# Performance work log

Hardware: AMD Instinct MI355X
Metric: run time of the kernel (lower is better)

## Reference

```python
import jax, jax.numpy as jnp
import numpy as np

NBATCH, NATOM, NEIGH = 16, 512, 64
NTYPE, NWAVE, NIPSIN, NORBIT = 4, 8, 3, 128
CUTOFF = 5.0
NPAIR = NATOM * NEIGH  # neighbor pairs per configuration


def _make_index_para(nipsin):
    # [0, 1,1,1, 2,...(9 times)] -> angular-order label per channel
    parts = [np.zeros(1, np.int32)]
    for i in range(1, nipsin):
        parts.append(np.full(3 ** i, i, np.int32))
    return jnp.asarray(np.concatenate(parts))


def setup_inputs() -> dict:
    key = jax.random.key(0)
    ks = jax.random.split(key, 10)
    cart = jax.random.uniform(ks[0], (NBATCH, NATOM, 3), jnp.float32) * 6.0
    numatoms = jnp.full((NBATCH,), NATOM, dtype=jnp.int32)
    species = jax.random.randint(ks[1], (NBATCH * NATOM,), 0, NTYPE).astype(jnp.int32)
    atom_index = jax.random.randint(ks[2], (2, NBATCH, NPAIR), 0, NATOM).astype(jnp.int32)
    shifts = jnp.zeros((NBATCH, NPAIR, 3), jnp.float32)  # all pairs valid (pass >-1e10 check)
    # learned parameters / buffers
    rs = jnp.tile(jnp.linspace(0.5, 4.0, NWAVE, dtype=jnp.float32)[None, :], (NTYPE, 1))
    inta = -(jax.random.uniform(ks[3], (NTYPE, NWAVE), jnp.float32) * 0.9 + 0.1)
    params = jnp.ones((NTYPE, NWAVE), jnp.float32) / float(NEIGH)
    hyper = jax.random.normal(ks[4], (1, NIPSIN, NWAVE, NORBIT), jnp.float32) * (1.0 / np.sqrt(NWAVE))
    index_para = _make_index_para(NIPSIN)
    return {"cart": cart, "numatoms": numatoms, "species": species,
            "atom_index": atom_index, "shifts": shifts,
            "rs": rs, "inta": inta, "params": params, "hyper": hyper,
            "index_para": index_para, "cutoff": CUTOFF}


def _angular(dist_vec, f_cut, nipsin):
    # dist_vec: [N,3], f_cut: [N] -> [L, N] with L = 1 + 3 + ... + 3^(nipsin-1)
    dv = dist_vec.T  # [3, N]
    orb = f_cut[None, :]
    parts = [orb]
    for _ in range(1, nipsin):
        orb = (orb[:, None, :] * dv[None, :, :]).reshape(-1, dv.shape[1])
        parts.append(orb)
    return jnp.concatenate(parts, axis=0)


def reference(cart, numatoms, species, atom_index, shifts, rs, inta, params, hyper, index_para, cutoff):
    nbatch, natom, _ = cart.shape
    totnatom = nbatch * natom
    cart_ = cart.reshape(totnatom, 3)
    # offset per-config neighbor indices to global atom ids
    offs = (jnp.arange(nbatch, dtype=atom_index.dtype) * natom)[None, :, None]
    idx12 = (atom_index + offs).reshape(2, -1)  # [2, Npairs]
    dist_vec = cart_[idx12[0]] - cart_[idx12[1]] + shifts.reshape(-1, 3)  # [Npairs,3]
    distances = jnp.linalg.norm(dist_vec, axis=-1)  # [Npairs]
    sp_j = species[idx12[1]]
    f_cut = jnp.square(0.5 * jnp.cos(distances * (jnp.pi / cutoff)) + 0.5)
    # per-pair gaussian radial basis, gathered by neighbor element type
    radial = jnp.exp(inta[sp_j] * jnp.square(distances[:, None] - rs[sp_j]))  # [Npairs, nwave]
    ang = _angular(dist_vec, f_cut, NIPSIN)  # [L, Npairs]
    orbital = ang.T[:, :, None] * radial[:, None, :]  # [Npairs, L, nwave]
    orb_coeff = params[species]  # [totnatom, nwave] (all species >= 0)
    # iteration 0 (ocmod_list is empty, so no refinement loop)
    worb = orbital * orb_coeff[idx12[1]][:, None, :]  # [Npairs, L, nwave]
    sum_worb = jax.ops.segment_sum(worb, idx12[0], num_segments=totnatom)  # [totnatom, L, nwave]
    hp = hyper[0][index_para]  # [L, nwave, norbit]
    hw = jnp.einsum('ijk,jkm->ijm', sum_worb, hp)  # [totnatom, L, norbit]
    density = jnp.sum(jnp.square(hw), axis=1)  # [totnatom, norbit]
    return density
```

## Files before the change

kernel.cpp:

```cpp
#include <hip/hip_runtime.h>
#include <hip/hip_bf16.h>

#define NBATCH  16
#define NATOM   512
#define NEIGH   64
#define NPAIR   (NATOM * NEIGH)
#define TOTPAIR (NBATCH * NPAIR)
#define TOTATOM (NBATCH * NATOM)
#define NTYPE   4
#define NWAVE   8
#define NL      13
#define NORBIT  128
#define CAP     128
#define NSUB    8
#define SUBCAP  40
#define PAIRS_PER_SUB (NPAIR / NSUB)

#define AST     136
#define S2ST    40

#define WS_COUNT_OFF 0
#define WS_HFRAG_OFF 262144
#define WS_PAY_OFF   278528


typedef __attribute__((ext_vector_type(8))) short  short8;
typedef __attribute__((ext_vector_type(4))) float  f32x4;

static __device__ inline unsigned short f2bf(float f) {
    unsigned u = __builtin_bit_cast(unsigned, f);
    u += 0x7FFFu + ((u >> 16) & 1u);
    return (unsigned short)(u >> 16);
}
static __device__ inline float bf2f(unsigned short h) {
    unsigned u = ((unsigned)h) << 16;
    return __builtin_bit_cast(float, u);
}

__global__ __launch_bounds__(512) void fill_kernel(
    const float* __restrict__ cart,
    const int*   __restrict__ species,
    const int*   __restrict__ atom_index,
    const float* __restrict__ shifts,
    const float* __restrict__ rs,
    const float* __restrict__ inta,
    const float* __restrict__ params,
    const float* __restrict__ cutoff_p,
    const float* __restrict__ hyper,
    int*            __restrict__ count,
    unsigned short* __restrict__ hfrag,
    unsigned short* __restrict__ payload)
{
    const int bid = blockIdx.x;
    const int b   = bid >> 3;
    const int s   = bid & 7;
    const int tid = threadIdx.x;

    __shared__ int   s_cnt[NATOM];
    __shared__ float s_tab[3 * NTYPE * NWAVE];

    if (tid < NTYPE * NWAVE) {
        s_tab[tid]                     = rs[tid];
        s_tab[NTYPE * NWAVE + tid]     = inta[tid];
        s_tab[2 * NTYPE * NWAVE + tid] = params[tid];
    }
    s_cnt[tid] = 0;

    if (bid < 16 && tid < 64) {
        const int hs = bid >> 3, n = bid & 7, lane = tid;
        const int q = lane >> 4, col = n * 16 + (lane & 15);
#pragma unroll
        for (int j = 0; j < 8; ++j) {
            int k = q * 8 + j;
            float f = (k < 24)
                ? hyper[(k >> 3) * (NWAVE * NORBIT) + (k & 7) * NORBIT + col]
                : 0.0f;
            unsigned short hi = f2bf(f);
            unsigned short v  = hs ? f2bf(f - bf2f(hi)) : hi;
            hfrag[((size_t)(bid * 64 + lane)) * 8 + j] = v;
        }
    }
    __syncthreads();

    const float pic = 3.14159265358979323846f / cutoff_p[0];
    const int pbase = b * NPAIR;

    for (int it = 0; it < PAIRS_PER_SUB / 512; ++it) {
        int pl = s * PAIRS_PER_SUB + it * 512 + tid;
        int p  = pbase + pl;
        int il = atom_index[p];
        int j  = atom_index[TOTPAIR + p] + (b << 9);
        int i  = il + (b << 9);

        float dx = cart[3 * i + 0] - cart[3 * j + 0] + shifts[3 * p + 0];
        float dy = cart[3 * i + 1] - cart[3 * j + 1] + shifts[3 * p + 1];
        float dz = cart[3 * i + 2] - cart[3 * j + 2] + shifts[3 * p + 2];
        float d  = sqrtf(dx * dx + dy * dy + dz * dz);

        float c  = 0.5f * __cosf(d * pic) + 0.5f;
        float fc = c * c;

        int slot = atomicAdd(&s_cnt[il], 1);
        if (slot < SUBCAP) {
            float a1 = fc * dx, a2 = fc * dy, a3 = fc * dz;
            short8 v0, v1, v2, v3;
            v0[0] = (short)f2bf(fc);
            v0[1] = (short)f2bf(a1);      v0[2] = (short)f2bf(a2);
            v0[3] = (short)f2bf(a3);
            v0[4] = (short)f2bf(a1 * dx); v0[5] = (short)f2bf(a1 * dy);
            v0[6] = (short)f2bf(a1 * dz); v0[7] = (short)f2bf(a2 * dx);
            v1[0] = (short)f2bf(a2 * dy); v1[1] = (short)f2bf(a2 * dz);
            v1[2] = (short)f2bf(a3 * dx); v1[3] = (short)f2bf(a3 * dy);
            v1[4] = (short)f2bf(a3 * dz);
            v1[5] = 0; v1[6] = 0; v1[7] = 0;

            int sp = species[j];
#pragma unroll
            for (int w = 0; w < NWAVE; ++w) {
                float tt = d - s_tab[sp * NWAVE + w];
                float rp = __expf(s_tab[NTYPE * NWAVE + sp * NWAVE + w] * tt * tt)
                         * s_tab[2 * NTYPE * NWAVE + sp * NWAVE + w];
                unsigned short hi = f2bf(rp);
                v2[w] = (short)hi;
                v3[w] = (short)f2bf(rp - bf2f(hi));
            }

            short8* dst = (short8*)(payload +
                (((size_t)((b * NATOM + il) * NSUB + s)) * SUBCAP + slot) * 32);
            dst[0] = v0; dst[1] = v1; dst[2] = v2; dst[3] = v3;
        }
    }
    __syncthreads();

    count[s * TOTATOM + (b * NATOM + tid)] = s_cnt[tid];
}

__global__ __launch_bounds__(128) void gather_kernel(
    const int*            __restrict__ count,
    const unsigned short* __restrict__ payload,
    const unsigned short* __restrict__ hfrag,
    float*                __restrict__ out)
{
    const int i      = blockIdx.x;
    const int tid    = threadIdx.x;
    const int lane   = tid & 63;
    const int waveId = tid >> 6;

    __shared__ __attribute__((aligned(16))) unsigned short s_A[16 * AST];
    __shared__ __attribute__((aligned(16))) unsigned short s_B[16 * AST];
    __shared__ __attribute__((aligned(16))) unsigned short s_S2[16 * S2ST];
    __shared__ int s_cv[NSUB];
    __shared__ int s_off[NSUB + 1];

    short8 hb[4], lb[4];
#pragma unroll
    for (int t = 0; t < 4; ++t) {
        int n = waveId * 4 + t;
        hb[t] = *(const short8*)&hfrag[((size_t)(n * 64 + lane)) * 8];
        lb[t] = *(const short8*)&hfrag[((size_t)((8 + n) * 64 + lane)) * 8];
    }

    if (tid < NSUB) {
        int c = count[tid * TOTATOM + i];
        s_cv[tid] = c < SUBCAP ? c : SUBCAP;
    }
    for (int e = tid; e < 16 * S2ST; e += 128) s_S2[e] = 0;
    __syncthreads();

    if (tid == 0) {
        int o = 0;
#pragma unroll
        for (int s2 = 0; s2 < NSUB; ++s2) { s_off[s2] = o; o += s_cv[s2]; }
        s_off[NSUB] = o;
    }
    __syncthreads();

    int total = s_off[NSUB];
    if (total > CAP) total = CAP;
    const int T = (total + 31) >> 5;

    if (tid < total) {
        const int k = tid;
        int s2 = 0;
#pragma unroll
        for (int t = 1; t < NSUB; ++t)
            if (k >= s_off[t]) s2 = t;
        const short8* rec = (const short8*)(payload +
            (((size_t)(i * NSUB + s2)) * SUBCAP + (k - s_off[s2])) * 32);
        short8 v0 = rec[0], v1 = rec[1], v2 = rec[2], v3 = rec[3];

        s_A[0 * AST + k]  = (unsigned short)v0[0];
        s_A[1 * AST + k]  = (unsigned short)v0[1];
        s_A[2 * AST + k]  = (unsigned short)v0[2];
        s_A[3 * AST + k]  = (unsigned short)v0[3];
        s_A[4 * AST + k]  = (unsigned short)v0[4];
        s_A[5 * AST + k]  = (unsigned short)v0[5];
        s_A[6 * AST + k]  = (unsigned short)v0[6];
        s_A[7 * AST + k]  = (unsigned short)v0[7];
        s_A[8 * AST + k]  = (unsigned short)v1[0];
        s_A[9 * AST + k]  = (unsigned short)v1[1];
        s_A[10 * AST + k] = (unsigned short)v1[2];
        s_A[11 * AST + k] = (unsigned short)v1[3];
        s_A[12 * AST + k] = (unsigned short)v1[4];
#pragma unroll
        for (int w = 0; w < NWAVE; ++w) {
            s_B[w * AST + k]       = (unsigned short)v2[w];
            s_B[(8 + w) * AST + k] = (unsigned short)v3[w];
        }
    }
    if (T > 0 && total < T * 32) {
        int tb = (T - 1) << 5;
        for (int e = tid; e < 16 * 32; e += 128) {
            int row = e >> 5, k = tb + (e & 31);
            if (k >= total) { s_A[row * AST + k] = 0; s_B[row * AST + k] = 0; }
        }
    }
    __syncthreads();

    if (waveId == 0) {
        const int m = lane & 15, q = lane >> 4;
        f32x4 acc = {0.f, 0.f, 0.f, 0.f};
        for (int t = 0; t < T; ++t) {
            short8 af  = *(const short8*)&s_A[m * AST + t * 32 + q * 8];
            short8 bhf = *(const short8*)&s_B[m * AST + t * 32 + q * 8];
            short8 blf = *(const short8*)&s_B[(m + 8) * AST + t * 32 + q * 8];
            acc = __builtin_amdgcn_mfma_f32_16x16x32_bf16(af, bhf, acc, 0, 0, 0);
            acc = __builtin_amdgcn_mfma_f32_16x16x32_bf16(af, blf, acc, 0, 0, 0);
        }
        if (m < 8) {
#pragma unroll
            for (int reg = 0; reg < 4; ++reg) {
                int l = q * 4 + reg;
                if (l < 13) {
                    int ip = (l == 0) ? 0 : ((l < 4) ? 1 : 2);
                    s_S2[l * S2ST + ip * 8 + m] = f2bf(acc[reg]);
                }
            }
        }
    }
    __syncthreads();

    {
        const int m = lane & 15, q = lane >> 4;
        short8 sf = *(const short8*)&s_S2[m * S2ST + q * 8];
#pragma unroll
        for (int t = 0; t < 4; ++t) {
            f32x4 acc = {0.f, 0.f, 0.f, 0.f};
            acc = __builtin_amdgcn_mfma_f32_16x16x32_bf16(sf, hb[t], acc, 0, 0, 0);
            acc = __builtin_amdgcn_mfma_f32_16x16x32_bf16(sf, lb[t], acc, 0, 0, 0);
            float part = 0.f;
#pragma unroll
            for (int reg = 0; reg < 4; ++reg) {
                int l = q * 4 + reg;
                if (l < 13) part += acc[reg] * acc[reg];
            }
            part += __shfl_xor(part, 16);
            part += __shfl_xor(part, 32);
            if (lane < 16)
                out[(size_t)i * NORBIT + (waveId * 4 + t) * 16 + lane] = part;
        }
    }
}

extern "C" void kernel_launch(void* const* d_in, const int* in_sizes, int n_in,
                              void* d_out, int out_size, void* d_ws, size_t ws_size,
                              hipStream_t stream) {
    const float* cart       = (const float*)d_in[0];
    const int*   species    = (const int*)  d_in[2];
    const int*   atom_index = (const int*)  d_in[3];
    const float* shifts     = (const float*)d_in[4];
    const float* rs         = (const float*)d_in[5];
    const float* inta       = (const float*)d_in[6];
    const float* params     = (const float*)d_in[7];
    const float* hyper      = (const float*)d_in[8];
    const float* cutoff_p   = (const float*)d_in[10];

    int*            count   = (int*)((char*)d_ws + WS_COUNT_OFF);
    unsigned short* hfrag   = (unsigned short*)((char*)d_ws + WS_HFRAG_OFF);
    unsigned short* payload = (unsigned short*)((char*)d_ws + WS_PAY_OFF);
    float* out = (float*)d_out;

    fill_kernel<<<NBATCH * NSUB, 512, 0, stream>>>(
        cart, species, atom_index, shifts, rs, inta, params, cutoff_p, hyper,
        count, hfrag, payload);

    gather_kernel<<<TOTATOM, 128, 0, stream>>>(count, payload, hfrag, out);
}
```

Before: 114.6 us.

## Process one atom per wave in gather and split fill into 16 sub-blocks

The fill kernel now uses 16 sub-blocks per batch with a smaller per-sub capacity, which doubles the fill grid so more CUs take part. The gather kernel is restructured so each 64-lane wave handles one atom on its own. It computes the sub-block offsets with a wave shuffle prefix scan instead of shared memory and __syncthreads, and it runs both MFMA stages inside that one wave. The hyper fragments are loaded per iteration from global memory instead of being held in registers, and payload and count workspace grows. The smaller SUBCAP (24 per sub) also changes when pairs overflow and get dropped.

```diff
diff --git a/kernel.cpp b/kernel.cpp
--- a/kernel.cpp
+++ b/kernel.cpp
@@ -12,16 +12,16 @@
 #define NL      13
 #define NORBIT  128
 #define CAP     128
-#define NSUB    8
-#define SUBCAP  40
+#define NSUB    16
+#define SUBCAP  24
 #define PAIRS_PER_SUB (NPAIR / NSUB)
 
 #define AST     136
 #define S2ST    40
 
 #define WS_COUNT_OFF 0
-#define WS_HFRAG_OFF 262144
-#define WS_PAY_OFF   278528
+#define WS_HFRAG_OFF 524288
+#define WS_PAY_OFF   540672
 
 
 typedef __attribute__((ext_vector_type(8))) short  short8;
@@ -52,8 +52,8 @@
     unsigned short* __restrict__ payload)
 {
     const int bid = blockIdx.x;
-    const int b   = bid >> 3;
-    const int s   = bid & 7;
+    const int b   = bid >> 4;
+    const int s   = bid & 15;
     const int tid = threadIdx.x;
 
     __shared__ int   s_cnt[NATOM];
@@ -77,7 +77,7 @@
                 : 0.0f;
             unsigned short hi = f2bf(f);
             unsigned short v  = hs ? f2bf(f - bf2f(hi)) : hi;
-            hfrag[((size_t)(bid * 64 + lane)) * 8 + j] = v;
+            hfrag[((size_t)(((hs << 3) | n) * 64 + lane)) * 8 + j] = v;
         }
     }
     __syncthreads();
@@ -85,6 +85,7 @@
     const float pic = 3.14159265358979323846f / cutoff_p[0];
     const int pbase = b * NPAIR;
 
+#pragma unroll
     for (int it = 0; it < PAIRS_PER_SUB / 512; ++it) {
         int pl = s * PAIRS_PER_SUB + it * 512 + tid;
         int p  = pbase + pl;
@@ -135,95 +136,89 @@
     count[s * TOTATOM + (b * NATOM + tid)] = s_cnt[tid];
 }
 
-__global__ __launch_bounds__(128) void gather_kernel(
+__global__ __launch_bounds__(256) void gather_kernel(
     const int*            __restrict__ count,
     const unsigned short* __restrict__ payload,
     const unsigned short* __restrict__ hfrag,
     float*                __restrict__ out)
 {
-    const int i      = blockIdx.x;
-    const int tid    = threadIdx.x;
-    const int lane   = tid & 63;
-    const int waveId = tid >> 6;
-
-    __shared__ __attribute__((aligned(16))) unsigned short s_A[16 * AST];
-    __shared__ __attribute__((aligned(16))) unsigned short s_B[16 * AST];
-    __shared__ __attribute__((aligned(16))) unsigned short s_S2[16 * S2ST];
-    __shared__ int s_cv[NSUB];
-    __shared__ int s_off[NSUB + 1];
-
-    short8 hb[4], lb[4];
-#pragma unroll
-    for (int t = 0; t < 4; ++t) {
-        int n = waveId * 4 + t;
-        hb[t] = *(const short8*)&hfrag[((size_t)(n * 64 + lane)) * 8];
-        lb[t] = *(const short8*)&hfrag[((size_t)((8 + n) * 64 + lane)) * 8];
-    }
-
-    if (tid < NSUB) {
-        int c = count[tid * TOTATOM + i];
-        s_cv[tid] = c < SUBCAP ? c : SUBCAP;
-    }
-    for (int e = tid; e < 16 * S2ST; e += 128) s_S2[e] = 0;
-    __syncthreads();
-
-    if (tid == 0) {
-        int o = 0;
-#pragma unroll
-        for (int s2 = 0; s2 < NSUB; ++s2) { s_off[s2] = o; o += s_cv[s2]; }
-        s_off[NSUB] = o;
-    }
-    __syncthreads();
-
-    int total = s_off[NSUB];
+    const int w    = threadIdx.x >> 6;
+    const int lane = threadIdx.x & 63;
+    const int i    = blockIdx.x * 4 + w;
+
+    __shared__ __attribute__((aligned(16))) unsigned short s_A [4][16 * AST];
+    __shared__ __attribute__((aligned(16))) unsigned short s_B [4][16 * AST];
+    __shared__ __attribute__((aligned(16))) unsigned short s_S2[4][16 * S2ST];
+
+    unsigned short* A  = s_A[w];
+    unsigned short* B  = s_B[w];
+    unsigned short* S2 = s_S2[w];
+
+    int c = 0;
+    if (lane < 16) {
+        c = count[lane * TOTATOM + i];
+        c = c < SUBCAP ? c : SUBCAP;
+    }
+    int inc = c;
+#pragma unroll
+    for (int d = 1; d < 16; d <<= 1) {
+        int t = __shfl_up(inc, d);
+        if (lane >= d && lane < 16) inc += t;
+    }
+    int excl = inc - c;
+    int off[16];
+#pragma unroll
+    for (int t = 0; t < 16; ++t) off[t] = __shfl(excl, t);
+    int total = __shfl(inc, 15);
     if (total > CAP) total = CAP;
     const int T = (total + 31) >> 5;
 
-    if (tid < total) {
-        const int k = tid;
+    for (int e = lane; e < 16 * S2ST; e += 64) S2[e] = 0;
+
+    for (int k = lane; k < total; k += 64) {
         int s2 = 0;
 #pragma unroll
-        for (int t = 1; t < NSUB; ++t)
-            if (k >= s_off[t]) s2 = t;
+        for (int t = 1; t < 16; ++t)
+            if (k >= off[t]) s2 = t;
         const short8* rec = (const short8*)(payload +
-            (((size_t)(i * NSUB + s2)) * SUBCAP + (k - s_off[s2])) * 32);
+            (((size_t)(i * NSUB + s2)) * SUBCAP + (k - off[s2])) * 32);
         short8 v0 = rec[0], v1 = rec[1], v2 = rec[2], v3 = rec[3];
 
-        s_A[0 * AST + k]  = (unsigned short)v0[0];
-        s_A[1 * AST + k]  = (unsigned short)v0[1];
-        s_A[2 * AST + k]  = (unsigned short)v0[2];
-        s_A[3 * AST + k]  = (unsigned short)v0[3];
-        s_A[4 * AST + k]  = (unsigned short)v0[4];
-        s_A[5 * AST + k]  = (unsigned short)v0[5];
-        s_A[6 * AST + k]  = (unsigned short)v0[6];
-        s_A[7 * AST + k]  = (unsigned short)v0[7];
-        s_A[8 * AST + k]  = (unsigned short)v1[0];
-        s_A[9 * AST + k]  = (unsigned short)v1[1];
-        s_A[10 * AST + k] = (unsigned short)v1[2];
-        s_A[11 * AST + k] = (unsigned short)v1[3];
-        s_A[12 * AST + k] = (unsigned short)v1[4];
-#pragma unroll
-        for (int w = 0; w < NWAVE; ++w) {
-            s_B[w * AST + k]       = (unsigned short)v2[w];
-            s_B[(8 + w) * AST + k] = (unsigned short)v3[w];
+        A[0 * AST + k]  = (unsigned short)v0[0];
+        A[1 * AST + k]  = (unsigned short)v0[1];
+        A[2 * AST + k]  = (unsigned short)v0[2];
+        A[3 * AST + k]  = (unsigned short)v0[3];
+        A[4 * AST + k]  = (unsigned short)v0[4];
+        A[5 * AST + k]  = (unsigned short)v0[5];
+        A[6 * AST + k]  = (unsigned short)v0[6];
+        A[7 * AST + k]  = (unsigned short)v0[7];
+        A[8 * AST + k]  = (unsigned short)v1[0];
+        A[9 * AST + k]  = (unsigned short)v1[1];
+        A[10 * AST + k] = (unsigned short)v1[2];
+        A[11 * AST + k] = (unsigned short)v1[3];
+        A[12 * AST + k] = (unsigned short)v1[4];
+#pragma unroll
+        for (int ww = 0; ww < NWAVE; ++ww) {
+            B[ww * AST + k]       = (unsigned short)v2[ww];
+            B[(8 + ww) * AST + k] = (unsigned short)v3[ww];
         }
     }
     if (T > 0 && total < T * 32) {
         int tb = (T - 1) << 5;
-        for (int e = tid; e < 16 * 32; e += 128) {
+        for (int e = lane; e < 16 * 32; e += 64) {
             int row = e >> 5, k = tb + (e & 31);
-            if (k >= total) { s_A[row * AST + k] = 0; s_B[row * AST + k] = 0; }
-        }
-    }
-    __syncthreads();
-
-    if (waveId == 0) {
-        const int m = lane & 15, q = lane >> 4;
+            if (k >= total) { A[row * AST + k] = 0; B[row * AST + k] = 0; }
+        }
+    }
+
+    const int m = lane & 15, q = lane >> 4;
+
+    {
         f32x4 acc = {0.f, 0.f, 0.f, 0.f};
         for (int t = 0; t < T; ++t) {
-            short8 af  = *(const short8*)&s_A[m * AST + t * 32 + q * 8];
-            short8 bhf = *(const short8*)&s_B[m * AST + t * 32 + q * 8];
-            short8 blf = *(const short8*)&s_B[(m + 8) * AST + t * 32 + q * 8];
+            short8 af  = *(const short8*)&A[m * AST + t * 32 + q * 8];
+            short8 bhf = *(const short8*)&B[m * AST + t * 32 + q * 8];
+            short8 blf = *(const short8*)&B[(m + 8) * AST + t * 32 + q * 8];
             acc = __builtin_amdgcn_mfma_f32_16x16x32_bf16(af, bhf, acc, 0, 0, 0);
             acc = __builtin_amdgcn_mfma_f32_16x16x32_bf16(af, blf, acc, 0, 0, 0);
         }
@@ -233,21 +228,21 @@
                 int l = q * 4 + reg;
                 if (l < 13) {
                     int ip = (l == 0) ? 0 : ((l < 4) ? 1 : 2);
-                    s_S2[l * S2ST + ip * 8 + m] = f2bf(acc[reg]);
+                    S2[l * S2ST + ip * 8 + m] = f2bf(acc[reg]);
                 }
             }
         }
     }
-    __syncthreads();
 
     {
-        const int m = lane & 15, q = lane >> 4;
-        short8 sf = *(const short8*)&s_S2[m * S2ST + q * 8];
-#pragma unroll
-        for (int t = 0; t < 4; ++t) {
+        short8 sf = *(const short8*)&S2[m * S2ST + q * 8];
+#pragma unroll
+        for (int t = 0; t < 8; ++t) {
+            short8 hbt = *(const short8*)&hfrag[((size_t)(t * 64 + lane)) * 8];
+            short8 lbt = *(const short8*)&hfrag[((size_t)((8 + t) * 64 + lane)) * 8];
             f32x4 acc = {0.f, 0.f, 0.f, 0.f};
-            acc = __builtin_amdgcn_mfma_f32_16x16x32_bf16(sf, hb[t], acc, 0, 0, 0);
-            acc = __builtin_amdgcn_mfma_f32_16x16x32_bf16(sf, lb[t], acc, 0, 0, 0);
+            acc = __builtin_amdgcn_mfma_f32_16x16x32_bf16(sf, hbt, acc, 0, 0, 0);
+            acc = __builtin_amdgcn_mfma_f32_16x16x32_bf16(sf, lbt, acc, 0, 0, 0);
             float part = 0.f;
 #pragma unroll
             for (int reg = 0; reg < 4; ++reg) {
@@ -257,7 +252,7 @@
             part += __shfl_xor(part, 16);
             part += __shfl_xor(part, 32);
             if (lane < 16)
-                out[(size_t)i * NORBIT + (waveId * 4 + t) * 16 + lane] = part;
+                out[(size_t)i * NORBIT + t * 16 + lane] = part;
         }
     }
 }
@@ -284,5 +279,5 @@
         cart, species, atom_index, shifts, rs, inta, params, cutoff_p, hyper,
         count, hfrag, payload);
 
-    gather_kernel<<<TOTATOM, 128, 0, stream>>>(count, payload, hfrag, out);
-}
+    gather_kernel<<<TOTATOM / 4, 256, 0, stream>>>(count, payload, hfrag, out);
+}
```

After: 110.6 us. 1.04x faster.
